# Kernel optimization log

Hardware: AMD Instinct MI355X
Metric: run time of the kernel (lower is better)

The kernel has to match this reference:

```python
import jax, jax.numpy as jnp
import numpy as np

B, NLOC, F, H = 16384, 12, 512, 256

def setup_inputs() -> dict:
    key = jax.random.key(0)
    ks = jax.random.split(key, 8)
    s = lambda n: 1.0 / np.sqrt(n)
    return {
        "global_feature": jax.random.normal(ks[0], (B, F), jnp.float32),
        "local_features": jax.random.normal(ks[1], (B, NLOC, F), jnp.float32),
        "Wq": jax.random.normal(ks[2], (F, H), jnp.float32) * s(F),
        "bq": jnp.zeros((H,), jnp.float32),
        "Wk": jax.random.normal(ks[3], (F, H), jnp.float32) * s(F),
        "bk": jnp.zeros((H,), jnp.float32),
        "Wv": jax.random.normal(ks[4], (F, H), jnp.float32) * s(F),
        "bv": jnp.zeros((H,), jnp.float32),
        "w_dr": jax.random.normal(ks[5], (NLOC,), jnp.float32) * s(NLOC),  # Linear(12,1) weight
        "b_dr": jnp.zeros((), jnp.float32),
        "Wf": jax.random.normal(ks[6], (2 * H, F), jnp.float32) * s(2 * H),
        "bf": jnp.zeros((F,), jnp.float32),
    }

def reference(global_feature, local_features, Wq, bq, Wk, bk, Wv, bv, w_dr, b_dr, Wf, bf):
    scale = 1.0 / jnp.sqrt(jnp.float32(H))
    # dimension_reduction over the 12 local tokens: Linear(12 -> 1)
    lf_mean = jnp.einsum('bkf,k->bf', local_features, w_dr) + b_dr  # [B, F]
    # --- local queries attend to the single global token ---
    gk = global_feature @ Wk + bk                       # [B, H]
    gv = global_feature @ Wv + bv                       # [B, H]
    lq = local_features @ Wq + bq                       # [B, 12, H]
    s1 = (jnp.einsum('bkh,bh->bk', lq, gk) * scale)[..., None]  # [B, 12, 1]
    a1 = jax.nn.softmax(s1, axis=-1)                    # softmax over length-1 key axis
    weighted_global = a1 * gv[:, None, :]               # [B, 12, H]
    # --- global query attends over the 12 local tokens ---
    gq = global_feature @ Wq + bq                       # [B, H]
    lk = local_features @ Wk + bk                       # [B, 12, H]
    lv = local_features @ Wv + bv                       # [B, 12, H]
    s2 = jnp.einsum('bh,bkh->bk', gq, lk) * scale       # [B, 12]
    a2 = jax.nn.softmax(s2, axis=-1)
    local_to_global = jnp.einsum('bk,bkh->bh', a2, lv)  # [B, H]
    # pool the 12-token axis of the weighted global feature
    wg_mean = jnp.einsum('bkh,k->bh', weighted_global, w_dr) + b_dr  # [B, H]
    combined = jnp.concatenate([local_to_global, wg_mean], axis=-1)  # [B, 2H]
    fused = jax.nn.relu(combined @ Wf + bf) + lf_mean + global_feature  # [B, F]
    return fused
```

## Files before the change

### kernel.cpp

```cpp
#include <hip/hip_runtime.h>

#define NLOC 12
#define F_DIM 512
#define H_DIM 256

typedef float f4 __attribute__((ext_vector_type(4)));
typedef _Float16 half4 __attribute__((ext_vector_type(4)));
typedef _Float16 half8 __attribute__((ext_vector_type(8)));

#define OFF_W1   0ul
#define OFF_W2   (OFF_W1 + 512ul*512*2)
#define OFF_C1   (OFF_W2 + 512ul*1024*2)
#define OFF_CVEC (OFF_C1 + 2048ul)
#define OFF_ACAT (OFF_CVEC + 2048ul)
#define OFF_BASE (OFF_ACAT + 16384ul*1024*2)

__global__ void __launch_bounds__(256) precompute_w(
    const float* __restrict__ Wq, const float* __restrict__ Wk,
    const float* __restrict__ Wv, const float* __restrict__ Wf,
    const float* __restrict__ wdr,
    _Float16* __restrict__ W1, _Float16* __restrict__ W2)
{
    __shared__ float X[32][264];
    __shared__ float Y[32][264];
    const int mode = blockIdx.z;
    const int f0 = blockIdx.x * 32;
    const int j0 = blockIdx.y * 32;
    const int t = threadIdx.x;

    {
        const int r = t >> 3, cb = (t & 7) * 32;
        const float* ysrc = ((mode == 0) ? Wq : Wv) + (j0 + r) * H_DIM + cb;
#pragma unroll
        for (int u = 0; u < 32; u += 4)
            *(f4*)&Y[r][cb + u] = *(const f4*)(ysrc + u);
        if (mode == 0) {
            const float* xsrc = Wk + (f0 + r) * H_DIM + cb;
#pragma unroll
            for (int u = 0; u < 32; u += 4)
                *(f4*)&X[r][cb + u] = *(const f4*)(xsrc + u);
        }
    }
    if (mode != 0) {
        const int h = t;
        const int hoff = (mode == 2) ? H_DIM : 0;
        const float* xsrc = Wf + (long)(h + hoff) * F_DIM + f0;
        f4 v[8];
#pragma unroll
        for (int u = 0; u < 8; ++u) v[u] = *(const f4*)(xsrc + u * 4);
#pragma unroll
        for (int r = 0; r < 32; ++r) X[r][h] = v[r >> 2][r & 3];
    }
    __syncthreads();

    const int fy = t >> 4, jx = t & 15;
    float a00 = 0.f, a01 = 0.f, a10 = 0.f, a11 = 0.f;
#pragma unroll 8
    for (int h = 0; h < H_DIM; ++h) {
        float x0 = X[fy][h], x1 = X[fy + 16][h];
        float y0 = Y[jx][h], y1 = Y[jx + 16][h];
        a00 += x0 * y0; a01 += x0 * y1; a10 += x1 * y0; a11 += x1 * y1;
    }
    if (mode == 2) {
        float S = 0.f;
#pragma unroll
        for (int k = 0; k < NLOC; ++k) S += wdr[k];
        a00 *= S; a01 *= S; a10 *= S; a11 *= S;
    }
    if (mode == 0) {
        W1[(f0 + fy) * F_DIM + (j0 + jx)]             = (_Float16)a00;
        W1[(f0 + fy) * F_DIM + (j0 + jx + 16)]        = (_Float16)a01;
        W1[(f0 + fy + 16) * F_DIM + (j0 + jx)]        = (_Float16)a10;
        W1[(f0 + fy + 16) * F_DIM + (j0 + jx + 16)]   = (_Float16)a11;
    } else {
        const long co = (mode == 2) ? F_DIM : 0;
        W2[(long)(f0 + fy) * 1024 + co + (j0 + jx)]           = (_Float16)a00;
        W2[(long)(f0 + fy) * 1024 + co + (j0 + jx + 16)]      = (_Float16)a01;
        W2[(long)(f0 + fy + 16) * 1024 + co + (j0 + jx)]      = (_Float16)a10;
        W2[(long)(f0 + fy + 16) * 1024 + co + (j0 + jx + 16)] = (_Float16)a11;
    }
}

__global__ void __launch_bounds__(256) cvec_kernel(
    const float* __restrict__ Wk, const float* __restrict__ Wf,
    const float* __restrict__ bq, const float* __restrict__ bv,
    const float* __restrict__ wdr, const float* __restrict__ bdr,
    const float* __restrict__ bfv,
    float* __restrict__ c1, float* __restrict__ cvec)
{
    const int f = blockIdx.x * 256 + threadIdx.x;
    f4 a = {0.f, 0.f, 0.f, 0.f};
    const f4* wk4 = (const f4*)(Wk + (long)f * H_DIM);
    const f4* bq4 = (const f4*)bq;
#pragma unroll 4
    for (int h4 = 0; h4 < H_DIM / 4; ++h4) a += wk4[h4] * bq4[h4];
    c1[f] = a[0] + a[1] + a[2] + a[3];

    float s1 = 0.f, s2 = 0.f, s3 = 0.f;
#pragma unroll 4
    for (int h = 0; h < H_DIM; ++h) {
        float w1v = Wf[h * F_DIM + f];
        float w2v = Wf[(H_DIM + h) * F_DIM + f];
        float bvh = bv[h];
        s1 += bvh * w1v; s2 += bvh * w2v; s3 += w2v;
    }
    float S = 0.f;
#pragma unroll
    for (int k = 0; k < NLOC; ++k) S += wdr[k];
    cvec[f] = s1 + S * s2 + bdr[0] * s3 + bfv[f];
}

__global__ void __launch_bounds__(256) fused_local(
    const float* __restrict__ g, const float* __restrict__ loc,
    const _Float16* __restrict__ W1, const float* __restrict__ c1,
    const float* __restrict__ wdr, const float* __restrict__ bdr,
    _Float16* __restrict__ Acat, _Float16* __restrict__ base)
{
    __shared__ _Float16 G[32][520];
    __shared__ _Float16 T[32][520];
    __shared__ _Float16 Bs[128][40];
    const int tid = threadIdx.x;
    const int lane = tid & 63;
    const int wave = tid >> 6;
    const int quad = lane >> 4;
    const int l16 = lane & 15;
    const long m0 = (long)blockIdx.x * 32;

    {
        const int r = tid >> 3;
        const int cb = (tid & 7) * 8;
#pragma unroll
        for (int u = 0; u < 512; u += 64) {
            const float* src = g + (m0 + r) * F_DIM + cb + u;
            f4 v0 = *(const f4*)(src);
            f4 v1 = *(const f4*)(src + 4);
            half8 hv;
#pragma unroll
            for (int j = 0; j < 4; ++j) { hv[j] = (_Float16)v0[j]; hv[4 + j] = (_Float16)v1[j]; }
            *(half8*)&G[r][cb + u] = hv;
        }
    }
    __syncthreads();

    const int srB = tid >> 1, scB = (tid & 1) * 16;
    const int wn1 = wave * 32;
    for (int nt = 0; nt < 4; ++nt) {
        const int n0 = nt * 128;
        f4 acc[2][2] = {{{0.f,0.f,0.f,0.f},{0.f,0.f,0.f,0.f}},
                        {{0.f,0.f,0.f,0.f},{0.f,0.f,0.f,0.f}}};
        for (int k0 = 0; k0 < 512; k0 += 32) {
            const _Float16* wsrc = W1 + (n0 + srB) * F_DIM + k0 + scB;
            uint4 w0 = *(const uint4*)(wsrc);
            uint4 w1 = *(const uint4*)(wsrc + 8);
            *(uint4*)&Bs[srB][scB] = w0;
            *(uint4*)&Bs[srB][scB + 8] = w1;
            __syncthreads();
            half8 a0 = *(const half8*)&G[l16][k0 + quad * 8];
            half8 a1 = *(const half8*)&G[16 + l16][k0 + quad * 8];
            half8 b0 = *(const half8*)&Bs[wn1 + l16][quad * 8];
            half8 b1 = *(const half8*)&Bs[wn1 + 16 + l16][quad * 8];
            acc[0][0] = __builtin_amdgcn_mfma_f32_16x16x32_f16(a0, b0, acc[0][0], 0, 0, 0);
            acc[0][1] = __builtin_amdgcn_mfma_f32_16x16x32_f16(a0, b1, acc[0][1], 0, 0, 0);
            acc[1][0] = __builtin_amdgcn_mfma_f32_16x16x32_f16(a1, b0, acc[1][0], 0, 0, 0);
            acc[1][1] = __builtin_amdgcn_mfma_f32_16x16x32_f16(a1, b1, acc[1][1], 0, 0, 0);
            __syncthreads();
        }
#pragma unroll
        for (int ni = 0; ni < 2; ++ni) {
            const int col = n0 + wn1 + ni * 16 + l16;
            const float cv = c1[col];
#pragma unroll
            for (int mi = 0; mi < 2; ++mi)
#pragma unroll
                for (int i = 0; i < 4; ++i)
                    T[mi * 16 + quad * 4 + i][col] = (_Float16)(acc[mi][ni][i] + cv);
        }
    }
    __syncthreads();

    const int c0 = lane * 4;
    const int c1i = 256 + lane * 4;
    const float bd = bdr[0];
    float wv[NLOC];
#pragma unroll
    for (int k = 0; k < NLOC; ++k) wv[k] = wdr[k];

    for (int rr = 0; rr < 8; ++rr) {
        const int bl = wave * 8 + rr;
        const long b = m0 + bl;
        const float* lb = loc + b * (NLOC * F_DIM);

        f4 la[NLOC], lbv[NLOC];
#pragma unroll
        for (int k = 0; k < NLOC; ++k) {
            la[k]  = *(const f4*)(lb + k * F_DIM + c0);
            lbv[k] = *(const f4*)(lb + k * F_DIM + c1i);
        }
        f4 taf = __builtin_convertvector(*(const half4*)&T[bl][c0], f4);
        f4 tbf = __builtin_convertvector(*(const half4*)&T[bl][c1i], f4);

        float p[NLOC];
#pragma unroll
        for (int k = 0; k < NLOC; ++k) {
            f4 prod = la[k] * taf + lbv[k] * tbf;
            p[k] = prod[0] + prod[1] + prod[2] + prod[3];
        }
#pragma unroll
        for (int k = 0; k < NLOC; ++k) {
            float v = p[k];
            v += __shfl_xor(v, 1);
            v += __shfl_xor(v, 2);
            v += __shfl_xor(v, 4);
            v += __shfl_xor(v, 8);
            v += __shfl_xor(v, 16);
            v += __shfl_xor(v, 32);
            p[k] = v * 0.0625f;
        }
        float mx = p[0];
#pragma unroll
        for (int k = 1; k < NLOC; ++k) mx = fmaxf(mx, p[k]);
        float e[NLOC], s = 0.f;
#pragma unroll
        for (int k = 0; k < NLOC; ++k) { e[k] = expf(p[k] - mx); s += e[k]; }
        const float inv = 1.f / s;

        f4 pA = {0.f,0.f,0.f,0.f}, pB = {0.f,0.f,0.f,0.f};
        f4 fA = {0.f,0.f,0.f,0.f}, fB = {0.f,0.f,0.f,0.f};
#pragma unroll
        for (int k = 0; k < NLOC; ++k) {
            const float ak = e[k] * inv;
            const float wk = wv[k];
            pA += ak * la[k]; pB += ak * lbv[k];
            fA += wk * la[k]; fB += wk * lbv[k];
        }
        half4 gA = *(const half4*)&G[bl][c0];
        half4 gB = *(const half4*)&G[bl][c1i];
        fA += bd + __builtin_convertvector(gA, f4);
        fB += bd + __builtin_convertvector(gB, f4);

        *(half4*)(Acat + b * 1024 + c0)          = __builtin_convertvector(pA, half4);
        *(half4*)(Acat + b * 1024 + c1i)         = __builtin_convertvector(pB, half4);
        *(half4*)(Acat + b * 1024 + 512 + c0)    = gA;
        *(half4*)(Acat + b * 1024 + 512 + c1i)   = gB;
        *(half4*)(base + b * F_DIM + c0)         = __builtin_convertvector(fA, half4);
        *(half4*)(base + b * F_DIM + c1i)        = __builtin_convertvector(fB, half4);
    }
}

__global__ void __launch_bounds__(256) gemm_final(
    const _Float16* __restrict__ A, const _Float16* __restrict__ Bt,
    const float* __restrict__ cvec, const _Float16* __restrict__ base,
    float* __restrict__ out)
{
    __shared__ _Float16 As[64][40];
    __shared__ _Float16 Bs[128][40];
    const int tid = threadIdx.x;
    const int lane = tid & 63;
    const int wave = tid >> 6;
    const int quad = lane >> 4;
    const int l16 = lane & 15;
    const int wm = (wave & 1) * 32;
    const int wn = (wave >> 1) * 64;
    const long m0 = (long)blockIdx.x * 64;
    const int n0 = blockIdx.y * 128;
    const int srA = tid >> 2, scA = (tid & 3) * 8;
    const int srB = tid >> 1, scB = (tid & 1) * 16;

    f4 acc[2][4];
#pragma unroll
    for (int mi = 0; mi < 2; ++mi)
#pragma unroll
        for (int nj = 0; nj < 4; ++nj) acc[mi][nj] = (f4){0.f,0.f,0.f,0.f};

    for (int k0 = 0; k0 < 1024; k0 += 32) {
        uint4 av = *(const uint4*)(A + (m0 + srA) * 1024 + k0 + scA);
        const _Float16* bsrc = Bt + (long)(n0 + srB) * 1024 + k0 + scB;
        uint4 b0v = *(const uint4*)(bsrc);
        uint4 b1v = *(const uint4*)(bsrc + 8);
        *(uint4*)&As[srA][scA] = av;
        *(uint4*)&Bs[srB][scB] = b0v;
        *(uint4*)&Bs[srB][scB + 8] = b1v;
        __syncthreads();
        half8 a0 = *(const half8*)&As[wm + l16][quad * 8];
        half8 a1 = *(const half8*)&As[wm + 16 + l16][quad * 8];
        half8 bf[4];
#pragma unroll
        for (int nj = 0; nj < 4; ++nj)
            bf[nj] = *(const half8*)&Bs[wn + nj * 16 + l16][quad * 8];
#pragma unroll
        for (int nj = 0; nj < 4; ++nj) {
            acc[0][nj] = __builtin_amdgcn_mfma_f32_16x16x32_f16(a0, bf[nj], acc[0][nj], 0, 0, 0);
            acc[1][nj] = __builtin_amdgcn_mfma_f32_16x16x32_f16(a1, bf[nj], acc[1][nj], 0, 0, 0);
        }
        __syncthreads();
    }

#pragma unroll
    for (int mi = 0; mi < 2; ++mi)
#pragma unroll
        for (int nj = 0; nj < 4; ++nj) {
            const int col = n0 + wn + nj * 16 + l16;
            const float cv = cvec[col];
#pragma unroll
            for (int i = 0; i < 4; ++i) {
                const long row = m0 + wm + mi * 16 + quad * 4 + i;
                float v = acc[mi][nj][i] + cv;
                v = fmaxf(v, 0.f) + (float)base[row * F_DIM + col];
                out[row * F_DIM + col] = v;
            }
        }
}

extern "C" void kernel_launch(void* const* d_in, const int* in_sizes, int n_in,
                              void* d_out, int out_size, void* d_ws, size_t ws_size,
                              hipStream_t stream)
{
    (void)in_sizes; (void)n_in; (void)out_size; (void)ws_size;
    const float* gf  = (const float*)d_in[0];
    const float* loc = (const float*)d_in[1];
    const float* Wq  = (const float*)d_in[2];
    const float* bq  = (const float*)d_in[3];
    const float* Wk  = (const float*)d_in[4];
    const float* Wv  = (const float*)d_in[6];
    const float* bv  = (const float*)d_in[7];
    const float* wdr = (const float*)d_in[8];
    const float* bdr = (const float*)d_in[9];
    const float* Wf  = (const float*)d_in[10];
    const float* bfv = (const float*)d_in[11];
    float* out = (float*)d_out;

    char* ws = (char*)d_ws;
    _Float16* W1   = (_Float16*)(ws + OFF_W1);
    _Float16* W2   = (_Float16*)(ws + OFF_W2);
    float*    c1   = (float*)(ws + OFF_C1);
    float*    cvec = (float*)(ws + OFF_CVEC);
    _Float16* Acat = (_Float16*)(ws + OFF_ACAT);
    _Float16* base = (_Float16*)(ws + OFF_BASE);

    precompute_w<<<dim3(16, 16, 3), 256, 0, stream>>>(Wq, Wk, Wv, Wf, wdr, W1, W2);
    cvec_kernel<<<2, 256, 0, stream>>>(Wk, Wf, bq, bv, wdr, bdr, bfv, c1, cvec);
    fused_local<<<512, 256, 0, stream>>>(gf, loc, W1, c1, wdr, bdr, Acat, base);
    gemm_final<<<dim3(256, 4), 256, 0, stream>>>(Acat, W2, cvec, base, out);
}
```

Measured before the change: 704.8 us.

## Load weight fragments directly from global memory and double-buffer A tile

Both GEMM loops now read the weight (B) fragments straight from global/L2 into registers instead of staging them through shared memory. This removes the per-k-step LDS staging and one barrier in fused_local. gemm_final double-buffers the A tile in shared memory, prefetching the next slice while the MFMAs run, and fully unrolls the k loop. The global-token half of Acat is now written during the initial load rather than in the epilogue, and launch bounds request higher occupancy. The trade-off is uncoalesced, redundant global loads of B across waves and possible register pressure from the unrolling and occupancy hints.

New measurement: 719.7 us. 2.1% more time.

```diff
diff --git a/kernel.cpp b/kernel.cpp
--- a/kernel.cpp
+++ b/kernel.cpp
@@ -110,7 +110,7 @@
     cvec[f] = s1 + S * s2 + bdr[0] * s3 + bfv[f];
 }
 
-__global__ void __launch_bounds__(256) fused_local(
+__global__ void __launch_bounds__(256, 2) fused_local(
     const float* __restrict__ g, const float* __restrict__ loc,
     const _Float16* __restrict__ W1, const float* __restrict__ c1,
     const float* __restrict__ wdr, const float* __restrict__ bdr,
@@ -118,7 +118,6 @@
 {
     __shared__ _Float16 G[32][520];
     __shared__ _Float16 T[32][520];
-    __shared__ _Float16 Bs[128][40];
     const int tid = threadIdx.x;
     const int lane = tid & 63;
     const int wave = tid >> 6;
@@ -138,32 +137,28 @@
 #pragma unroll
             for (int j = 0; j < 4; ++j) { hv[j] = (_Float16)v0[j]; hv[4 + j] = (_Float16)v1[j]; }
             *(half8*)&G[r][cb + u] = hv;
+            *(half8*)(Acat + (m0 + r) * 1024 + 512 + cb + u) = hv;
         }
     }
     __syncthreads();
 
-    const int srB = tid >> 1, scB = (tid & 1) * 16;
     const int wn1 = wave * 32;
     for (int nt = 0; nt < 4; ++nt) {
         const int n0 = nt * 128;
+        const _Float16* wb0 = W1 + (long)(n0 + wn1 + l16) * F_DIM + quad * 8;
+        const _Float16* wb1 = wb0 + 16 * F_DIM;
         f4 acc[2][2] = {{{0.f,0.f,0.f,0.f},{0.f,0.f,0.f,0.f}},
                         {{0.f,0.f,0.f,0.f},{0.f,0.f,0.f,0.f}}};
+#pragma unroll
         for (int k0 = 0; k0 < 512; k0 += 32) {
-            const _Float16* wsrc = W1 + (n0 + srB) * F_DIM + k0 + scB;
-            uint4 w0 = *(const uint4*)(wsrc);
-            uint4 w1 = *(const uint4*)(wsrc + 8);
-            *(uint4*)&Bs[srB][scB] = w0;
-            *(uint4*)&Bs[srB][scB + 8] = w1;
-            __syncthreads();
+            half8 b0 = *(const half8*)(wb0 + k0);
+            half8 b1 = *(const half8*)(wb1 + k0);
             half8 a0 = *(const half8*)&G[l16][k0 + quad * 8];
             half8 a1 = *(const half8*)&G[16 + l16][k0 + quad * 8];
-            half8 b0 = *(const half8*)&Bs[wn1 + l16][quad * 8];
-            half8 b1 = *(const half8*)&Bs[wn1 + 16 + l16][quad * 8];
             acc[0][0] = __builtin_amdgcn_mfma_f32_16x16x32_f16(a0, b0, acc[0][0], 0, 0, 0);
             acc[0][1] = __builtin_amdgcn_mfma_f32_16x16x32_f16(a0, b1, acc[0][1], 0, 0, 0);
             acc[1][0] = __builtin_amdgcn_mfma_f32_16x16x32_f16(a1, b0, acc[1][0], 0, 0, 0);
             acc[1][1] = __builtin_amdgcn_mfma_f32_16x16x32_f16(a1, b1, acc[1][1], 0, 0, 0);
-            __syncthreads();
         }
 #pragma unroll
         for (int ni = 0; ni < 2; ++ni) {
@@ -240,20 +235,17 @@
 
         *(half4*)(Acat + b * 1024 + c0)          = __builtin_convertvector(pA, half4);
         *(half4*)(Acat + b * 1024 + c1i)         = __builtin_convertvector(pB, half4);
-        *(half4*)(Acat + b * 1024 + 512 + c0)    = gA;
-        *(half4*)(Acat + b * 1024 + 512 + c1i)   = gB;
         *(half4*)(base + b * F_DIM + c0)         = __builtin_convertvector(fA, half4);
         *(half4*)(base + b * F_DIM + c1i)        = __builtin_convertvector(fB, half4);
     }
 }
 
-__global__ void __launch_bounds__(256) gemm_final(
+__global__ void __launch_bounds__(256, 3) gemm_final(
     const _Float16* __restrict__ A, const _Float16* __restrict__ Bt,
     const float* __restrict__ cvec, const _Float16* __restrict__ base,
     float* __restrict__ out)
 {
-    __shared__ _Float16 As[64][40];
-    __shared__ _Float16 Bs[128][40];
+    __shared__ _Float16 As[2][64][40];
     const int tid = threadIdx.x;
     const int lane = tid & 63;
     const int wave = tid >> 6;
@@ -264,7 +256,12 @@
     const long m0 = (long)blockIdx.x * 64;
     const int n0 = blockIdx.y * 128;
     const int srA = tid >> 2, scA = (tid & 3) * 8;
-    const int srB = tid >> 1, scB = (tid & 1) * 16;
+
+    const _Float16* bp0 = Bt + (long)(n0 + wn + l16) * 1024 + quad * 8;
+    const _Float16* bp1 = bp0 + 16 * 1024;
+    const _Float16* bp2 = bp0 + 32 * 1024;
+    const _Float16* bp3 = bp0 + 48 * 1024;
+    const _Float16* ap  = A + (m0 + srA) * 1024 + scA;
 
     f4 acc[2][4];
 #pragma unroll
@@ -272,26 +269,29 @@
 #pragma unroll
         for (int nj = 0; nj < 4; ++nj) acc[mi][nj] = (f4){0.f,0.f,0.f,0.f};
 
-    for (int k0 = 0; k0 < 1024; k0 += 32) {
-        uint4 av = *(const uint4*)(A + (m0 + srA) * 1024 + k0 + scA);
-        const _Float16* bsrc = Bt + (long)(n0 + srB) * 1024 + k0 + scB;
-        uint4 b0v = *(const uint4*)(bsrc);
-        uint4 b1v = *(const uint4*)(bsrc + 8);
-        *(uint4*)&As[srA][scA] = av;
-        *(uint4*)&Bs[srB][scB] = b0v;
-        *(uint4*)&Bs[srB][scB + 8] = b1v;
-        __syncthreads();
-        half8 a0 = *(const half8*)&As[wm + l16][quad * 8];
-        half8 a1 = *(const half8*)&As[wm + 16 + l16][quad * 8];
-        half8 bf[4];
-#pragma unroll
-        for (int nj = 0; nj < 4; ++nj)
-            bf[nj] = *(const half8*)&Bs[wn + nj * 16 + l16][quad * 8];
-#pragma unroll
-        for (int nj = 0; nj < 4; ++nj) {
-            acc[0][nj] = __builtin_amdgcn_mfma_f32_16x16x32_f16(a0, bf[nj], acc[0][nj], 0, 0, 0);
-            acc[1][nj] = __builtin_amdgcn_mfma_f32_16x16x32_f16(a1, bf[nj], acc[1][nj], 0, 0, 0);
-        }
+    *(uint4*)&As[0][srA][scA] = *(const uint4*)(ap);
+    __syncthreads();
+
+#pragma unroll
+    for (int kt = 0; kt < 32; ++kt) {
+        const int k0 = kt * 32;
+        uint4 avn;
+        if (kt < 31) avn = *(const uint4*)(ap + k0 + 32);
+        half8 b0 = *(const half8*)(bp0 + k0);
+        half8 b1 = *(const half8*)(bp1 + k0);
+        half8 b2 = *(const half8*)(bp2 + k0);
+        half8 b3 = *(const half8*)(bp3 + k0);
+        half8 a0 = *(const half8*)&As[kt & 1][wm + l16][quad * 8];
+        half8 a1 = *(const half8*)&As[kt & 1][wm + 16 + l16][quad * 8];
+        acc[0][0] = __builtin_amdgcn_mfma_f32_16x16x32_f16(a0, b0, acc[0][0], 0, 0, 0);
+        acc[1][0] = __builtin_amdgcn_mfma_f32_16x16x32_f16(a1, b0, acc[1][0], 0, 0, 0);
+        acc[0][1] = __builtin_amdgcn_mfma_f32_16x16x32_f16(a0, b1, acc[0][1], 0, 0, 0);
+        acc[1][1] = __builtin_amdgcn_mfma_f32_16x16x32_f16(a1, b1, acc[1][1], 0, 0, 0);
+        acc[0][2] = __builtin_amdgcn_mfma_f32_16x16x32_f16(a0, b2, acc[0][2], 0, 0, 0);
+        acc[1][2] = __builtin_amdgcn_mfma_f32_16x16x32_f16(a1, b2, acc[1][2], 0, 0, 0);
+        acc[0][3] = __builtin_amdgcn_mfma_f32_16x16x32_f16(a0, b3, acc[0][3], 0, 0, 0);
+        acc[1][3] = __builtin_amdgcn_mfma_f32_16x16x32_f16(a1, b3, acc[1][3], 0, 0, 0);
+        if (kt < 31) *(uint4*)&As[(kt & 1) ^ 1][srA][scA] = avn;
         __syncthreads();
     }
 
```
